# Kernel tuning notes

Measured on AMD Instinct MI355X. Metric: run time of the kernel, lower is better.

The kernel has to match this reference:

```python
import jax, jax.numpy as jnp
import numpy as np

EPS = 1e-3  # nn.LayerNorm(eps=0.001)
PADDING = 0.0


def setup_inputs() -> dict:
    key = jax.random.key(0)
    k1, k2, k3, k4 = jax.random.split(key, 4)
    N, M, K3, C_IN, C_OUT, B = 200000, 40000, 27, 64, 128, 4
    features = jax.random.normal(k1, (N, C_IN), dtype=jnp.float32)
    center_coors = jax.random.normal(k2, (M, 3), dtype=jnp.float32)
    voxel_idx = jax.random.randint(k3, (M, K3), 0, N, dtype=jnp.int64)
    num_list = jnp.full((B,), M // B, dtype=jnp.int32)
    W = jax.random.normal(k4, (K3 * C_IN, C_OUT), dtype=jnp.float32) * 1e-4
    gamma = jnp.ones((C_OUT,), dtype=jnp.float32)
    beta = jnp.zeros((C_OUT,), dtype=jnp.float32)
    return {
        "features": features,
        "center_coors": center_coors,
        "voxel_idx": voxel_idx,
        "num_list": num_list,
        "W": W,
        "gamma": gamma,
        "beta": beta,
        "num_keypoints": 2048,
    }


def _block(features, voxel_idx, W, gamma, beta):
    M, K3 = voxel_idx.shape
    C_in = features.shape[1]
    # voxel neighbor gather; negative idx -> padding value
    gathered = features[jnp.clip(voxel_idx, 0, features.shape[0] - 1)]  # [M, K3, C_in]
    gathered = jnp.where(voxel_idx[..., None] < 0, PADDING, gathered)
    flat = gathered.reshape(M, K3 * C_in)
    out = flat @ W  # [M, C_out]
    # LayerNorm over channel dim (per-batch loop in torch is mathematically
    # identical to a single row-wise LayerNorm)
    mu = jnp.mean(out, axis=-1, keepdims=True)
    var = jnp.mean(jnp.square(out - mu), axis=-1, keepdims=True)
    out = (out - mu) / jnp.sqrt(var + EPS) * gamma + beta
    return jax.nn.relu(out)


def _resample(out_features, center_coors, num_list, num_keypoints):
    B = num_list.shape[0]
    K = num_keypoints
    accum = jnp.cumsum(num_list)
    offsets = jnp.concatenate([jnp.zeros((1,), accum.dtype), accum[:-1]])  # [B]
    j = jnp.arange(K, dtype=jnp.int32)  # [K]
    end = jnp.minimum(num_list, jnp.int32(K))  # [B]
    valid = j[None, :] < end[:, None]  # [B, K]
    src = jnp.clip(offsets[:, None] + j[None, :], 0, out_features.shape[0] - 1)  # [B, K]
    res_feat = jnp.where(valid[..., None], out_features[src], 0.0)  # [B, K, C]
    res_xyz = jnp.where(valid[..., None], center_coors[src], 0.0)  # [B, K, 3]
    # replicate original quirk: segments 0..B-2 get batch index 1..B-1, last stays 0
    bid = jnp.arange(B, dtype=jnp.float32)
    col0 = jnp.where(bid < B - 1, bid + 1.0, 0.0)  # [B]
    col0 = jnp.broadcast_to(col0[:, None, None], (B, K, 1))
    res_coor = jnp.concatenate([col0, res_xyz], axis=-1)  # [B, K, 4]
    C = out_features.shape[1]
    return res_feat.reshape(B * K, C), res_coor.reshape(B * K, 4)


def reference(features, center_coors, voxel_idx, num_list, W, gamma, beta, num_keypoints):
    out = _block(features, voxel_idx, W, gamma, beta)
    point_features, point_coords = _resample(out, center_coors, num_list, num_keypoints)
    return point_features, point_coords
```

## Files before the change

### kernel.cpp

```cpp
#include <hip/hip_runtime.h>
#include <hip/hip_bf16.h>
#include <stdint.h>
#include <stddef.h>

#define TM 16
#define CIN 64
#define NK3 27
#define COUT 128
#define EPS_LN 1e-3f
#define KCH (NK3 * CIN / 32)
#define NT  (COUT / 16)

typedef __attribute__((ext_vector_type(8))) short   short8;
typedef __attribute__((ext_vector_type(4))) float   floatx4;
typedef __attribute__((ext_vector_type(4))) unsigned short ushort4v;

__device__ __forceinline__ unsigned short f2b(float f) {
    union { float f; unsigned int i; } v;
    v.f = f;
    unsigned int i = v.i;
    return (unsigned short)((i + 0x7fffu + ((i >> 16) & 1u)) >> 16);
}

__global__ __launch_bounds__(256) void pack_w(const float* __restrict__ Wm,
                                              unsigned short* __restrict__ pk) {
    int slot = blockIdx.x * 256 + threadIdx.x;
    int l  = slot & 63;
    int kk = (slot >> 6) % KCH;
    int nt = slot / (64 * KCH);
    int q = l >> 4, n = l & 15;
    const float* src = Wm + (size_t)(kk * 32 + q * 8) * COUT + nt * 16 + n;
    short8 v;
    #pragma unroll
    for (int j = 0; j < 8; ++j)
        v[j] = (short)f2b(src[(size_t)j * COUT]);
    *(short8*)(pk + (size_t)slot * 8) = v;
}

__global__ __launch_bounds__(256) void dpc_mfma(
    const float* __restrict__ features,
    const float* __restrict__ center,
    const int* __restrict__ voxel_idx,
    const int* __restrict__ num_list,
    const unsigned short* __restrict__ pk,
    const float* __restrict__ gamma_,
    const float* __restrict__ beta_,
    float* __restrict__ out_feat,
    float* __restrict__ out_coor,
    int N, int M, int B, int K, int Rtot)
{
    __shared__ int s_flags;
    __shared__ int s_vid[TM][NK3];
    __shared__ int s_src[TM];
    __shared__ int s_valid[TM];
    __shared__ __align__(16) unsigned short s_a[2][1024];
    __shared__ float s_c[TM][COUT + 4];

    const int t  = threadIdx.x;
    const int R0 = blockIdx.x * TM;

    if (t == 0) {
        int f = 0;
        bool v64 = true;
        for (int j = 1; j < 128; j += 2) {
            if (voxel_idx[j] != 0) { v64 = false; break; }
        }
        if (v64) f |= 1;
        bool n64 = false;
        if (B >= 2) {
            n64 = (num_list[1] == 0) && (num_list[0] != 0);
            if (B >= 4) n64 = n64 && (num_list[3] == 0);
        }
        if (n64) f |= 2;
        s_flags = f;
    }
    __syncthreads();
    const bool vidx64 = (s_flags & 1) != 0;
    const bool nl64   = (s_flags & 2) != 0;

    if (t < TM) {
        int r = R0 + t;
        int src = 0, valid = 0;
        if (r < Rtot) {
            int b = r / K;
            int j = r - b * K;
            int offs = 0, nlb = 0;
            for (int i = 0; i < B; ++i) {
                int v = nl64 ? num_list[2 * i] : num_list[i];
                if (i < b) offs += v;
                if (i == b) nlb = v;
            }
            int end = nlb < K ? nlb : K;
            valid = (j < end) ? 1 : 0;
            src = offs + j;
            if (src < 0) src = 0;
            if (src > M - 1) src = M - 1;
        }
        s_src[t] = src;
        s_valid[t] = valid;
    }
    __syncthreads();

    if (t < TM * 4) {
        int i = t >> 2, comp = t & 3;
        int r = R0 + i;
        if (r < Rtot) {
            float val;
            if (comp == 0) {
                int b = r / K;
                val = (b < B - 1) ? (float)(b + 1) : 0.0f;
            } else {
                val = s_valid[i] ? center[(size_t)s_src[i] * 3 + comp - 1] : 0.0f;
            }
            out_coor[(size_t)r * 4 + comp] = val;
        }
    }

    for (int lin = t; lin < TM * NK3; lin += 256) {
        int i = lin / NK3;
        int k = lin - i * NK3;
        size_t e = (size_t)s_src[i] * NK3 + k;
        s_vid[i][k] = vidx64 ? voxel_idx[2 * e] : voxel_idx[e];
    }
    __syncthreads();

    const int m  = t >> 4;
    const int c0 = (t & 15) * 4;
    const int chunk = c0 >> 5;
    const int q4    = (c0 & 31) >> 3;
    const int j0    = c0 & 7;
    const int aoff  = chunk * 512 + (q4 * 16 + m) * 8 + j0;

    auto gatherf4 = [&](int kc) -> float4 {
        int idx = s_vid[m][kc];
        float4 r = make_float4(0.f, 0.f, 0.f, 0.f);
        if (idx >= 0) {
            if (idx > N - 1) idx = N - 1;
            r = *(const float4*)(features + (size_t)idx * CIN + c0);
        }
        return r;
    };
    auto stash = [&](int buf, float4 v) {
        ushort4v u;
        u[0] = f2b(v.x); u[1] = f2b(v.y); u[2] = f2b(v.z); u[3] = f2b(v.w);
        *(ushort4v*)&s_a[buf][aoff] = u;
    };

    const int w    = t >> 6;
    const int lane = t & 63;
    const int nt0 = 2 * w, nt1 = 2 * w + 1;

    floatx4 acc0 = {0.f, 0.f, 0.f, 0.f};
    floatx4 acc1 = {0.f, 0.f, 0.f, 0.f};

    stash(0, gatherf4(0));
    __syncthreads();

    for (int kc = 0; kc < NK3; ++kc) {
        float4 pref;
        const bool hn = (kc + 1 < NK3);
        if (hn) pref = gatherf4(kc + 1);

        const int kk0 = kc * 2;
        const int buf = kc & 1;
        const short8 b00 = *(const short8*)(pk + ((size_t)(nt0 * KCH + kk0    ) * 64 + lane) * 8);
        const short8 b01 = *(const short8*)(pk + ((size_t)(nt0 * KCH + kk0 + 1) * 64 + lane) * 8);
        const short8 b10 = *(const short8*)(pk + ((size_t)(nt1 * KCH + kk0    ) * 64 + lane) * 8);
        const short8 b11 = *(const short8*)(pk + ((size_t)(nt1 * KCH + kk0 + 1) * 64 + lane) * 8);
        const short8 a0 = *(const short8*)&s_a[buf][lane * 8];
        const short8 a1 = *(const short8*)&s_a[buf][512 + lane * 8];

        acc0 = __builtin_amdgcn_mfma_f32_16x16x32_bf16(a0, b00, acc0, 0, 0, 0);
        acc0 = __builtin_amdgcn_mfma_f32_16x16x32_bf16(a1, b01, acc0, 0, 0, 0);
        acc1 = __builtin_amdgcn_mfma_f32_16x16x32_bf16(a0, b10, acc1, 0, 0, 0);
        acc1 = __builtin_amdgcn_mfma_f32_16x16x32_bf16(a1, b11, acc1, 0, 0, 0);

        if (hn) stash((kc + 1) & 1, pref);
        __syncthreads();
    }

    {
        const int q = lane >> 4, n = lane & 15;
        #pragma unroll
        for (int reg = 0; reg < 4; ++reg) {
            s_c[q * 4 + reg][nt0 * 16 + n] = acc0[reg];
            s_c[q * 4 + reg][nt1 * 16 + n] = acc1[reg];
        }
    }
    __syncthreads();

    const int h  = t >> 6;
    const int c2 = (t & 63) * 2;
    const float g0  = gamma_[c2];
    const float g1  = gamma_[c2 + 1];
    const float be0 = beta_[c2];
    const float be1 = beta_[c2 + 1];

    #pragma unroll
    for (int i = 0; i < 4; ++i) {
        int row = h * 4 + i;
        float a0 = s_c[row][c2];
        float a1 = s_c[row][c2 + 1];
        float s  = a0 + a1;
        float ss = a0 * a0 + a1 * a1;
        #pragma unroll
        for (int mm = 1; mm < 64; mm <<= 1) {
            s  += __shfl_xor(s,  mm, 64);
            ss += __shfl_xor(ss, mm, 64);
        }
        float mu   = s * (1.0f / COUT);
        float var  = ss * (1.0f / COUT) - mu * mu;
        float rstd = rsqrtf(var + EPS_LN);
        float v0 = (a0 - mu) * rstd * g0 + be0;
        float v1 = (a1 - mu) * rstd * g1 + be1;
        v0 = fmaxf(v0, 0.f);
        v1 = fmaxf(v1, 0.f);
        if (!s_valid[row]) { v0 = 0.f; v1 = 0.f; }
        int r = R0 + row;
        if (r < Rtot) {
            out_feat[(size_t)r * COUT + c2]     = v0;
            out_feat[(size_t)r * COUT + c2 + 1] = v1;
        }
    }
}

extern "C" void kernel_launch(void* const* d_in, const int* in_sizes, int n_in,
                              void* d_out, int out_size, void* d_ws, size_t ws_size,
                              hipStream_t stream) {
    const float* features = (const float*)d_in[0];
    const float* center   = (const float*)d_in[1];
    const int*   vidx     = (const int*)d_in[2];
    const int*   num_list = (const int*)d_in[3];
    const float* Wm       = (const float*)d_in[4];
    const float* gamma_   = (const float*)d_in[5];
    const float* beta_    = (const float*)d_in[6];

    const int B    = in_sizes[3];
    const int Cout = in_sizes[5];
    const int M    = in_sizes[1] / 3;
    const int K3v  = in_sizes[2] / M;
    const int Cin  = (in_sizes[4] / Cout) / K3v;
    const int N    = in_sizes[0] / Cin;
    const int Rtot = out_size / (Cout + 4);
    const int K    = Rtot / B;

    float* out_feat = (float*)d_out;
    float* out_coor = out_feat + (size_t)Rtot * Cout;
    unsigned short* pk = (unsigned short*)d_ws;

    const int pack_grid = (NT * KCH * 64) / 256;
    pack_w<<<dim3(pack_grid), dim3(256), 0, stream>>>(Wm, pk);

    const int grid = (Rtot + TM - 1) / TM;
    dpc_mfma<<<dim3(grid), dim3(256), 0, stream>>>(
        features, center, vidx, num_list, pk, gamma_, beta_,
        out_feat, out_coor, N, M, B, K, Rtot);
}
```

Before: 115.0 us.

## Process kernel offsets in pairs with register-prefetched B fragments

Pads the 27 kernel offsets to 28 so the main loop handles two offsets per iteration. This halves the number of block-wide barriers and doubles the gather work in flight per iteration. The packed weight fragments for the next pair are now prefetched into registers one iteration ahead instead of loaded just before use. The cost is more registers, a doubled shared A buffer, and one wasted zero-padded offset of MFMA and weight-packing work.

```diff
diff --git a/kernel.cpp b/kernel.cpp
--- a/kernel.cpp
+++ b/kernel.cpp
@@ -6,10 +6,13 @@
 #define TM 16
 #define CIN 64
 #define NK3 27
+#define NK3P 28
 #define COUT 128
 #define EPS_LN 1e-3f
-#define KCH (NK3 * CIN / 32)
-#define NT  (COUT / 16)
+#define KCH  (NK3 * CIN / 32)
+#define KCHP (NK3P * CIN / 32)
+#define NT   (COUT / 16)
+#define NPAIR (NK3P / 2)
 
 typedef __attribute__((ext_vector_type(8))) short   short8;
 typedef __attribute__((ext_vector_type(4))) float   floatx4;
@@ -26,14 +29,16 @@
                                               unsigned short* __restrict__ pk) {
     int slot = blockIdx.x * 256 + threadIdx.x;
     int l  = slot & 63;
-    int kk = (slot >> 6) % KCH;
-    int nt = slot / (64 * KCH);
-    int q = l >> 4, n = l & 15;
-    const float* src = Wm + (size_t)(kk * 32 + q * 8) * COUT + nt * 16 + n;
-    short8 v;
-    #pragma unroll
-    for (int j = 0; j < 8; ++j)
-        v[j] = (short)f2b(src[(size_t)j * COUT]);
+    int kk = (slot >> 6) % KCHP;
+    int nt = slot / (64 * KCHP);
+    short8 v = {0, 0, 0, 0, 0, 0, 0, 0};
+    if (kk < KCH) {
+        int q = l >> 4, n = l & 15;
+        const float* src = Wm + (size_t)(kk * 32 + q * 8) * COUT + nt * 16 + n;
+        #pragma unroll
+        for (int j = 0; j < 8; ++j)
+            v[j] = (short)f2b(src[(size_t)j * COUT]);
+    }
     *(short8*)(pk + (size_t)slot * 8) = v;
 }
 
@@ -50,10 +55,10 @@
     int N, int M, int B, int K, int Rtot)
 {
     __shared__ int s_flags;
-    __shared__ int s_vid[TM][NK3];
+    __shared__ int s_vid[TM][NK3P];
     __shared__ int s_src[TM];
     __shared__ int s_valid[TM];
-    __shared__ __align__(16) unsigned short s_a[2][1024];
+    __shared__ __align__(16) unsigned short s_a[2][2048];
     __shared__ float s_c[TM][COUT + 4];
 
     const int t  = threadIdx.x;
@@ -116,11 +121,15 @@
         }
     }
 
-    for (int lin = t; lin < TM * NK3; lin += 256) {
-        int i = lin / NK3;
-        int k = lin - i * NK3;
-        size_t e = (size_t)s_src[i] * NK3 + k;
-        s_vid[i][k] = vidx64 ? voxel_idx[2 * e] : voxel_idx[e];
+    for (int lin = t; lin < TM * NK3P; lin += 256) {
+        int i = lin / NK3P;
+        int k = lin - i * NK3P;
+        int v = -1;
+        if (k < NK3) {
+            size_t e = (size_t)s_src[i] * NK3 + k;
+            v = vidx64 ? voxel_idx[2 * e] : voxel_idx[e];
+        }
+        s_vid[i][k] = v;
     }
     __syncthreads();
 
@@ -140,43 +149,71 @@
         }
         return r;
     };
-    auto stash = [&](int buf, float4 v) {
+    auto stash = [&](int buf, int sub, float4 v) {
         ushort4v u;
         u[0] = f2b(v.x); u[1] = f2b(v.y); u[2] = f2b(v.z); u[3] = f2b(v.w);
-        *(ushort4v*)&s_a[buf][aoff] = u;
+        *(ushort4v*)&s_a[buf][sub * 1024 + aoff] = u;
     };
 
     const int w    = t >> 6;
     const int lane = t & 63;
     const int nt0 = 2 * w, nt1 = 2 * w + 1;
 
+    auto loadB = [&](int nt, int kk) -> short8 {
+        return *(const short8*)(pk + ((size_t)(nt * KCHP + kk) * 64 + lane) * 8);
+    };
+
     floatx4 acc0 = {0.f, 0.f, 0.f, 0.f};
     floatx4 acc1 = {0.f, 0.f, 0.f, 0.f};
 
-    stash(0, gatherf4(0));
-    __syncthreads();
-
-    for (int kc = 0; kc < NK3; ++kc) {
-        float4 pref;
-        const bool hn = (kc + 1 < NK3);
-        if (hn) pref = gatherf4(kc + 1);
-
-        const int kk0 = kc * 2;
-        const int buf = kc & 1;
-        const short8 b00 = *(const short8*)(pk + ((size_t)(nt0 * KCH + kk0    ) * 64 + lane) * 8);
-        const short8 b01 = *(const short8*)(pk + ((size_t)(nt0 * KCH + kk0 + 1) * 64 + lane) * 8);
-        const short8 b10 = *(const short8*)(pk + ((size_t)(nt1 * KCH + kk0    ) * 64 + lane) * 8);
-        const short8 b11 = *(const short8*)(pk + ((size_t)(nt1 * KCH + kk0 + 1) * 64 + lane) * 8);
-        const short8 a0 = *(const short8*)&s_a[buf][lane * 8];
-        const short8 a1 = *(const short8*)&s_a[buf][512 + lane * 8];
-
-        acc0 = __builtin_amdgcn_mfma_f32_16x16x32_bf16(a0, b00, acc0, 0, 0, 0);
-        acc0 = __builtin_amdgcn_mfma_f32_16x16x32_bf16(a1, b01, acc0, 0, 0, 0);
-        acc1 = __builtin_amdgcn_mfma_f32_16x16x32_bf16(a0, b10, acc1, 0, 0, 0);
-        acc1 = __builtin_amdgcn_mfma_f32_16x16x32_bf16(a1, b11, acc1, 0, 0, 0);
-
-        if (hn) stash((kc + 1) & 1, pref);
+    stash(0, 0, gatherf4(0));
+    stash(0, 1, gatherf4(1));
+    short8 bb[8];
+    #pragma unroll
+    for (int c = 0; c < 4; ++c) {
+        bb[2 * c]     = loadB(nt0, c);
+        bb[2 * c + 1] = loadB(nt1, c);
+    }
+    __syncthreads();
+
+    for (int p = 0; p < NPAIR; ++p) {
+        const int  buf = p & 1;
+        const bool hn  = (p + 1 < NPAIR);
+
+        float4 n0, n1;
+        if (hn) { n0 = gatherf4(2 * p + 2); n1 = gatherf4(2 * p + 3); }
+        short8 nb[8];
+        if (hn) {
+            #pragma unroll
+            for (int c = 0; c < 4; ++c) {
+                nb[2 * c]     = loadB(nt0, 4 * (p + 1) + c);
+                nb[2 * c + 1] = loadB(nt1, 4 * (p + 1) + c);
+            }
+        }
+
+        const short8 a0 = *(const short8*)&s_a[buf][           lane * 8];
+        const short8 a1 = *(const short8*)&s_a[buf][ 512 +     lane * 8];
+        const short8 a2 = *(const short8*)&s_a[buf][1024 +     lane * 8];
+        const short8 a3 = *(const short8*)&s_a[buf][1536 +     lane * 8];
+
+        acc0 = __builtin_amdgcn_mfma_f32_16x16x32_bf16(a0, bb[0], acc0, 0, 0, 0);
+        acc1 = __builtin_amdgcn_mfma_f32_16x16x32_bf16(a0, bb[1], acc1, 0, 0, 0);
+        acc0 = __builtin_amdgcn_mfma_f32_16x16x32_bf16(a1, bb[2], acc0, 0, 0, 0);
+        acc1 = __builtin_amdgcn_mfma_f32_16x16x32_bf16(a1, bb[3], acc1, 0, 0, 0);
+        acc0 = __builtin_amdgcn_mfma_f32_16x16x32_bf16(a2, bb[4], acc0, 0, 0, 0);
+        acc1 = __builtin_amdgcn_mfma_f32_16x16x32_bf16(a2, bb[5], acc1, 0, 0, 0);
+        acc0 = __builtin_amdgcn_mfma_f32_16x16x32_bf16(a3, bb[6], acc0, 0, 0, 0);
+        acc1 = __builtin_amdgcn_mfma_f32_16x16x32_bf16(a3, bb[7], acc1, 0, 0, 0);
+
+        if (hn) {
+            stash(buf ^ 1, 0, n0);
+            stash(buf ^ 1, 1, n1);
+        }
         __syncthreads();
+        if (hn) {
+            #pragma unroll
+            for (int i = 0; i < 8; ++i) bb[i] = nb[i];
+        }
     }
 
     {
@@ -248,7 +285,7 @@
     float* out_coor = out_feat + (size_t)Rtot * Cout;
     unsigned short* pk = (unsigned short*)d_ws;
 
-    const int pack_grid = (NT * KCH * 64) / 256;
+    const int pack_grid = (NT * KCHP * 64) / 256;
     pack_w<<<dim3(pack_grid), dim3(256), 0, stream>>>(Wm, pk);
 
     const int grid = (Rtot + TM - 1) / TM;
```

Measured after the change: 113.2 us. Within noise of the previous version (-1.5%).
